# Optimization experiments

Measured on AMD Instinct MI355X. Metric: run time of the kernel, lower is better.

## Reference

```python
import jax, jax.numpy as jnp
import numpy as np

N = 100000
E = 3200000
IN_DIM = 512
OUT_DIM = 128


def setup_inputs() -> dict:
    key = jax.random.key(0)
    k1, k2, k3 = jax.random.split(key, 3)
    x = jax.random.normal(k1, (N, IN_DIM), dtype=jnp.float32)
    edge_index = jax.random.randint(k2, (2, E), 0, N, dtype=jnp.int64)
    # Glorot init like PyG GCNConv
    W = jax.random.normal(k3, (IN_DIM, OUT_DIM), dtype=jnp.float32) * (2.0 / (IN_DIM + OUT_DIM)) ** 0.5
    b = jnp.zeros((OUT_DIM,), dtype=jnp.float32)
    return {"x": x, "edge_index": edge_index, "W": W, "b": b}


def gcn_conv(x, edge_index, W, b):
    # GCNConv with add_self_loops=True, normalize=True (symmetric norm)
    row, col = edge_index[0], edge_index[1]  # messages flow row -> col
    xw = x @ W  # [N, out_dim]
    ones = jnp.ones((E,), dtype=xw.dtype)
    # degree of destination nodes, +1 for self-loop
    deg = jax.ops.segment_sum(ones, col, num_segments=N) + 1.0
    dinv = jax.lax.rsqrt(deg)  # deg^{-1/2}, deg >= 1 so no inf
    norm = dinv[row] * dinv[col]  # [E]
    msg = xw[row] * norm[:, None]  # gather + scale
    out = jax.ops.segment_sum(msg, col, num_segments=N)  # scatter-add
    # self-loop contribution: norm_ii = dinv_i * dinv_i
    out = out + xw * (dinv * dinv)[:, None]
    return out + b


def reference(x, edge_index, W, b):
    return gcn_conv(x, edge_index, W, b)
```

## Files before the change

kernel.cpp:

```cpp
#include <hip/hip_runtime.h>

using short8  = __attribute__((ext_vector_type(8))) short;
using f32x4   = __attribute__((ext_vector_type(4))) float;
using uint32x4 = __attribute__((ext_vector_type(4))) unsigned;

static constexpr int N_NODES = 100000;
static constexpr int N_EDGES = 3200000;
static constexpr int IN_DIM  = 512;
static constexpr int OUT_DIM = 128;
static constexpr int NBINS   = (N_NODES + 255) / 256;
static constexpr int NB      = 1024;
static constexpr int CHUNK   = N_EDGES / NB;

__device__ __forceinline__ short f2bf(float f) {
  unsigned u = __builtin_bit_cast(unsigned, f);
  u = (u + 0x7FFFu + ((u >> 16) & 1u)) >> 16;
  return (short)u;
}

__global__ __launch_bounds__(256) void cast_WT(const float* __restrict__ W,
                                               short* __restrict__ WTb) {
  const int idx = blockIdx.x * 256 + threadIdx.x;
  const int k = idx >> 7, c = idx & 127;
  const int ks = k >> 5, lk = (k >> 3) & 3, j = k & 7;
  WTb[(size_t)((ks * 128 + c) * 4 + lk) * 8 + j] = f2bf(W[(size_t)k * 128 + c]);
}

__global__ __launch_bounds__(256, 4) void gemm_direct(const float* __restrict__ x,
                                                      const short* __restrict__ WTb,
                                                      const float* __restrict__ dinv,
                                                      unsigned short* __restrict__ xwb) {
  const int tid = threadIdx.x;
  const int w   = tid >> 6;
  const int l   = tid & 63;
  const int lr  = l & 15;
  const int lk  = l >> 4;
  const int row0 = blockIdx.x * 64 + w * 16;

  const int ra = min(row0 + lr, N_NODES - 1);
  const float* pa = &x[(size_t)ra * IN_DIM + lk * 8];
  const char*  wb = reinterpret_cast<const char*>(WTb) + lr * 64 + lk * 16;

  f32x4 acc[8] = {};

  float4 A0[2], A1[2];
  short8 B[2][8];

  auto loadA = [&](int ks, int s) {
    const float* p = pa + ks * 32;
    A0[s] = *reinterpret_cast<const float4*>(p);
    A1[s] = *reinterpret_cast<const float4*>(p + 4);
  };
  auto loadB = [&](int ks, int s) {
    const char* base = wb + ks * 8192;
#pragma unroll
    for (int cf = 0; cf < 8; ++cf)
      B[s][cf] = *reinterpret_cast<const short8*>(base + cf * 1024);
  };
  auto cvt2 = [](float lo, float hi) -> unsigned {
    unsigned r;
    asm("v_cvt_pk_bf16_f32 %0, %1, %2" : "=v"(r) : "v"(lo), "v"(hi));
    return r;
  };
  auto compute = [&](int s) {
    uint32x4 ua;
    ua[0] = cvt2(A0[s].x, A0[s].y);
    ua[1] = cvt2(A0[s].z, A0[s].w);
    ua[2] = cvt2(A1[s].x, A1[s].y);
    ua[3] = cvt2(A1[s].z, A1[s].w);
    const short8 a = __builtin_bit_cast(short8, ua);
#pragma unroll
    for (int cf = 0; cf < 8; ++cf)
      acc[cf] = __builtin_amdgcn_mfma_f32_16x16x32_bf16(a, B[s][cf], acc[cf], 0, 0, 0);
  };

  loadA(0, 0);
  loadB(0, 0);

#pragma unroll
  for (int kp = 0; kp < 8; ++kp) {
    const int ks = kp * 2;
    loadA(ks + 1, 1);
    loadB(ks + 1, 1);
    compute(0);
    if (kp < 7) {
      loadA(ks + 2, 0);
      loadB(ks + 2, 0);
    }
    compute(1);
  }

#pragma unroll
  for (int j = 0; j < 4; ++j) {
    const int row = row0 + lk * 4 + j;
    if (row < N_NODES) {
      const float sc = dinv[row];
      unsigned short* o = &xwb[(size_t)row * OUT_DIM + lr];
#pragma unroll
      for (int cf = 0; cf < 8; ++cf)
        o[cf * 16] = (unsigned short)f2bf(acc[cf][j] * sc);
    }
  }
}


__global__ __launch_bounds__(256) void bin_count(const int* __restrict__ ecol,
                                                 int* __restrict__ blkhist) {
  __shared__ int hist[NBINS];
  const int blk = blockIdx.x, tid = threadIdx.x;
  for (int i = tid; i < NBINS; i += 256) hist[i] = 0;
  __syncthreads();
  const int e0 = blk * CHUNK, e1 = e0 + CHUNK;
  for (int e = e0 + tid; e < e1; e += 256) atomicAdd(&hist[ecol[e] >> 8], 1);
  __syncthreads();
  for (int i = tid; i < NBINS; i += 256) blkhist[(size_t)blk * NBINS + i] = hist[i];
}

__global__ __launch_bounds__(1024) void scan_blkhist(int* __restrict__ blkhist,
                                                     int* __restrict__ bintot) {
  __shared__ int sh[NB];
  const int bin = blockIdx.x, t = threadIdx.x;
  const int v = blkhist[(size_t)t * NBINS + bin];
  sh[t] = v;
  __syncthreads();
  for (int d = 1; d < NB; d <<= 1) {
    const int tv = (t >= d) ? sh[t - d] : 0;
    __syncthreads();
    sh[t] += tv;
    __syncthreads();
  }
  blkhist[(size_t)t * NBINS + bin] = sh[t] - v;
  if (t == NB - 1) bintot[bin] = sh[t];
}

__global__ __launch_bounds__(512) void scan_bins(const int* __restrict__ bintot,
                                                 int* __restrict__ binbase) {
  __shared__ int sh[512];
  const int t = threadIdx.x;
  const int v = (t < NBINS) ? bintot[t] : 0;
  sh[t] = v;
  __syncthreads();
  for (int d = 1; d < 512; d <<= 1) {
    const int tv = (t >= d) ? sh[t - d] : 0;
    __syncthreads();
    sh[t] += tv;
    __syncthreads();
  }
  if (t < NBINS) binbase[t] = sh[t] - v;
  if (t == NBINS - 1) binbase[NBINS] = sh[t];
}

__global__ __launch_bounds__(256) void bin_scatter(const int* __restrict__ erow,
                                                   const int* __restrict__ ecol,
                                                   const int* __restrict__ blkhist,
                                                   const int* __restrict__ binbase,
                                                   unsigned* __restrict__ benc) {
  __shared__ int cur[NBINS];
  const int blk = blockIdx.x, tid = threadIdx.x;
  for (int i = tid; i < NBINS; i += 256)
    cur[i] = binbase[i] + blkhist[(size_t)blk * NBINS + i];
  __syncthreads();
  const int e0 = blk * CHUNK, e1 = e0 + CHUNK;
  for (int e = e0 + tid; e < e1; e += 256) {
    const int c = ecol[e];
    const unsigned enc = (unsigned)erow[e] | ((unsigned)(c & 255) << 24);
    const int p = atomicAdd(&cur[c >> 8], 1);
    benc[p] = enc;
  }
}

__global__ __launch_bounds__(256) void bin_build(const unsigned* __restrict__ benc,
                                                 const int* __restrict__ binbase,
                                                 int* __restrict__ brow,
                                                 int* __restrict__ offs,
                                                 float* __restrict__ dinv) {
  __shared__ int hist[256];
  __shared__ int sh[256];
  __shared__ int cur[256];
  const int b = blockIdx.x, tid = threadIdx.x;
  const int e0 = binbase[b], e1 = binbase[b + 1];
  hist[tid] = 0;
  __syncthreads();
  for (int e = e0 + tid; e < e1; e += 256) atomicAdd(&hist[benc[e] >> 24], 1);
  __syncthreads();
  const int d0 = hist[tid];
  sh[tid] = d0;
  __syncthreads();
  for (int d = 1; d < 256; d <<= 1) {
    const int tv = (tid >= d) ? sh[tid - d] : 0;
    __syncthreads();
    sh[tid] += tv;
    __syncthreads();
  }
  const int myoff = e0 + sh[tid] - d0;
  cur[tid] = myoff;
  const int node = (b << 8) + tid;
  if (node < N_NODES) {
    offs[node] = myoff;
    dinv[node] = rsqrtf((float)d0 + 1.0f);
  }
  if (b == NBINS - 1 && tid == 255) offs[N_NODES] = e1;
  __syncthreads();
  for (int e = e0 + tid; e < e1; e += 256) {
    const unsigned v = benc[e];
    const int p = atomicAdd(&cur[v >> 24], 1);
    brow[p] = (int)(v & 0x00FFFFFFu);
  }
}

__global__ __launch_bounds__(256) void gather_out(const unsigned short* __restrict__ xwb,
                                                  const float* __restrict__ dinv,
                                                  const int* __restrict__ offs,
                                                  const int* __restrict__ brow,
                                                  const float* __restrict__ bias,
                                                  float* __restrict__ out) {
  const int lane = threadIdx.x & 63;
  const int node = blockIdx.x * (blockDim.x >> 6) + (threadIdx.x >> 6);
  if (node >= N_NODES) return;
  const float di = dinv[node];
  const int c0 = lane * 2;

  auto ld2 = [&](int r) -> float2 {
    const unsigned v = *reinterpret_cast<const unsigned*>(&xwb[(size_t)r * OUT_DIM + c0]);
    float2 f;
    f.x = __builtin_bit_cast(float, v << 16);
    f.y = __builtin_bit_cast(float, v & 0xFFFF0000u);
    return f;
  };

  float2 acc = ld2(node);

  int e = offs[node];
  const int e1 = offs[node + 1];
  for (; e + 8 <= e1; e += 8) {
    const int r0 = brow[e],     r1 = brow[e + 1], r2 = brow[e + 2], r3 = brow[e + 3];
    const int r4 = brow[e + 4], r5 = brow[e + 5], r6 = brow[e + 6], r7 = brow[e + 7];
    const float2 v0 = ld2(r0), v1 = ld2(r1), v2 = ld2(r2), v3 = ld2(r3);
    const float2 v4 = ld2(r4), v5 = ld2(r5), v6 = ld2(r6), v7 = ld2(r7);
    acc.x += ((v0.x + v1.x) + (v2.x + v3.x)) + ((v4.x + v5.x) + (v6.x + v7.x));
    acc.y += ((v0.y + v1.y) + (v2.y + v3.y)) + ((v4.y + v5.y) + (v6.y + v7.y));
  }
  for (; e < e1; ++e) {
    const float2 v = ld2(brow[e]);
    acc.x += v.x;
    acc.y += v.y;
  }

  const float2 bb = *reinterpret_cast<const float2*>(&bias[c0]);
  float2 o;
  o.x = acc.x * di + bb.x;
  o.y = acc.y * di + bb.y;
  *reinterpret_cast<float2*>(&out[(size_t)node * OUT_DIM + c0]) = o;
}

extern "C" void kernel_launch(void* const* d_in, const int* in_sizes, int n_in,
                              void* d_out, int out_size, void* d_ws, size_t ws_size,
                              hipStream_t stream) {
  const float* x    = (const float*)d_in[0];
  const int*   eidx = (const int*)d_in[1];
  const float* W    = (const float*)d_in[2];
  const float* b    = (const float*)d_in[3];
  float* out = (float*)d_out;

  const int* erow = eidx;
  const int* ecol = eidx + N_EDGES;

  char* ws = (char*)d_ws;
  size_t off = 0;
  auto alloc = [&](size_t bytes) -> void* {
    void* p = ws + off;
    off = (off + bytes + 255) & ~(size_t)255;
    return p;
  };
  unsigned short* xwb = (unsigned short*)alloc((size_t)N_NODES * OUT_DIM * sizeof(short));
  short* WTb     = (short*)alloc((size_t)OUT_DIM * IN_DIM * sizeof(short));
  float* dinv    = (float*)alloc((size_t)N_NODES * sizeof(float));
  int*   offs    = (int*)alloc((size_t)(N_NODES + 1) * sizeof(int));
  int*   blkhist = (int*)alloc((size_t)NB * NBINS * sizeof(int));
  int*   bintot  = (int*)alloc((size_t)NBINS * sizeof(int));
  int*   binbase = (int*)alloc((size_t)(NBINS + 1) * sizeof(int));
  int*   brow    = (int*)alloc((size_t)N_EDGES * sizeof(int));
  unsigned* benc = (unsigned*)alloc((size_t)N_EDGES * sizeof(unsigned));

  cast_WT<<<256, 256, 0, stream>>>(W, WTb);

  bin_count<<<NB, 256, 0, stream>>>(ecol, blkhist);
  scan_blkhist<<<NBINS, NB, 0, stream>>>(blkhist, bintot);
  scan_bins<<<1, 512, 0, stream>>>(bintot, binbase);
  bin_scatter<<<NB, 256, 0, stream>>>(erow, ecol, blkhist, binbase, benc);
  bin_build<<<NBINS, 256, 0, stream>>>(benc, binbase, brow, offs, dinv);

  gemm_direct<<<(N_NODES + 63) / 64, 256, 0, stream>>>(x, WTb, dinv, xwb);
  gather_out<<<(N_NODES + 3) / 4, 256, 0, stream>>>(xwb, dinv, offs, brow, b, out);
}
```

Measured before the change: 309.0 us.

## Slice bf16 XW into 16-column planes and gather per slice

The GEMM output is stored as 8 column slices of 16 bf16 values per node instead of full rows. The gather kernel now assigns 8 lanes per node per slice, with 8 blocks per node group, one for each slice. Each slice is smaller, which is meant to improve cache locality for the random row gathers. In exchange, the edge list and offsets are read 8 times, and each gathered access becomes a narrow 32-byte segment.

```diff
diff --git a/kernel.cpp b/kernel.cpp
--- a/kernel.cpp
+++ b/kernel.cpp
@@ -95,10 +95,10 @@
     const int row = row0 + lk * 4 + j;
     if (row < N_NODES) {
       const float sc = dinv[row];
-      unsigned short* o = &xwb[(size_t)row * OUT_DIM + lr];
 #pragma unroll
       for (int cf = 0; cf < 8; ++cf)
-        o[cf * 16] = (unsigned short)f2bf(acc[cf][j] * sc);
+        xwb[((size_t)cf * N_NODES + row) * 16 + lr] =
+            (unsigned short)f2bf(acc[cf][j] * sc);
     }
   }
 }
@@ -214,14 +214,23 @@
                                                   const int* __restrict__ brow,
                                                   const float* __restrict__ bias,
                                                   float* __restrict__ out) {
-  const int lane = threadIdx.x & 63;
-  const int node = blockIdx.x * (blockDim.x >> 6) + (threadIdx.x >> 6);
+  const int bid   = blockIdx.x;
+  const int slice = bid & 7;
+  const int chunk = bid >> 3;
+  const int tid   = threadIdx.x;
+  const int wave  = tid >> 6;
+  const int lane  = tid & 63;
+  const int sub   = lane >> 3;
+  const int sl    = lane & 7;
+  const int node  = chunk * 32 + wave * 8 + sub;
   if (node >= N_NODES) return;
+
+  const unsigned short* xs = xwb + (size_t)slice * N_NODES * 16;
   const float di = dinv[node];
-  const int c0 = lane * 2;
+  const int c0 = sl * 2;
 
   auto ld2 = [&](int r) -> float2 {
-    const unsigned v = *reinterpret_cast<const unsigned*>(&xwb[(size_t)r * OUT_DIM + c0]);
+    const unsigned v = *reinterpret_cast<const unsigned*>(&xs[(size_t)r * 16 + c0]);
     float2 f;
     f.x = __builtin_bit_cast(float, v << 16);
     f.y = __builtin_bit_cast(float, v & 0xFFFF0000u);
@@ -232,13 +241,11 @@
 
   int e = offs[node];
   const int e1 = offs[node + 1];
-  for (; e + 8 <= e1; e += 8) {
-    const int r0 = brow[e],     r1 = brow[e + 1], r2 = brow[e + 2], r3 = brow[e + 3];
-    const int r4 = brow[e + 4], r5 = brow[e + 5], r6 = brow[e + 6], r7 = brow[e + 7];
+  for (; e + 4 <= e1; e += 4) {
+    const int r0 = brow[e], r1 = brow[e + 1], r2 = brow[e + 2], r3 = brow[e + 3];
     const float2 v0 = ld2(r0), v1 = ld2(r1), v2 = ld2(r2), v3 = ld2(r3);
-    const float2 v4 = ld2(r4), v5 = ld2(r5), v6 = ld2(r6), v7 = ld2(r7);
-    acc.x += ((v0.x + v1.x) + (v2.x + v3.x)) + ((v4.x + v5.x) + (v6.x + v7.x));
-    acc.y += ((v0.y + v1.y) + (v2.y + v3.y)) + ((v4.y + v5.y) + (v6.y + v7.y));
+    acc.x += (v0.x + v1.x) + (v2.x + v3.x);
+    acc.y += (v0.y + v1.y) + (v2.y + v3.y);
   }
   for (; e < e1; ++e) {
     const float2 v = ld2(brow[e]);
@@ -246,11 +253,12 @@
     acc.y += v.y;
   }
 
-  const float2 bb = *reinterpret_cast<const float2*>(&bias[c0]);
+  const int oc = slice * 16 + c0;
+  const float2 bb = *reinterpret_cast<const float2*>(&bias[oc]);
   float2 o;
   o.x = acc.x * di + bb.x;
   o.y = acc.y * di + bb.y;
-  *reinterpret_cast<float2*>(&out[(size_t)node * OUT_DIM + c0]) = o;
+  *reinterpret_cast<float2*>(&out[(size_t)node * OUT_DIM + oc]) = o;
 }
 
 extern "C" void kernel_launch(void* const* d_in, const int* in_sizes, int n_in,
@@ -272,7 +280,7 @@
     off = (off + bytes + 255) & ~(size_t)255;
     return p;
   };
-  unsigned short* xwb = (unsigned short*)alloc((size_t)N_NODES * OUT_DIM * sizeof(short));
+  unsigned short* xwb = (unsigned short*)alloc((size_t)8 * N_NODES * 16 * sizeof(short));
   short* WTb     = (short*)alloc((size_t)OUT_DIM * IN_DIM * sizeof(short));
   float* dinv    = (float*)alloc((size_t)N_NODES * sizeof(float));
   int*   offs    = (int*)alloc((size_t)(N_NODES + 1) * sizeof(int));
@@ -291,5 +299,5 @@
   bin_build<<<NBINS, 256, 0, stream>>>(benc, binbase, brow, offs, dinv);
 
   gemm_direct<<<(N_NODES + 63) / 64, 256, 0, stream>>>(x, WTb, dinv, xwb);
-  gather_out<<<(N_NODES + 3) / 4, 256, 0, stream>>>(xwb, dinv, offs, brow, b, out);
-}
+  gather_out<<<8 * ((N_NODES + 31) / 32), 256, 0, stream>>>(xwb, dinv, offs, brow, b, out);
+}
```

New measurement: 361.2 us. +16.9%, slower.
